# Performance work log

Hardware: AMD Instinct MI355X
Metric: run time of the kernel (lower is better)

## Reference

```python
import jax, jax.numpy as jnp
import numpy as np

TEMPERATURE = 1.0

def setup_inputs() -> dict:
    key = jax.random.key(0)
    k1, k2 = jax.random.split(key)
    B, I, O = 256, 1024, 1024
    x = jax.random.normal(k1, (B, I), dtype=jnp.float32)
    # mimic TruncatedNormal(stddev=1/sqrt(input_size)) init
    w = jax.random.normal(k2, (I, O), dtype=jnp.float32) * (1.0 / np.sqrt(I))
    b = jnp.zeros((O,), dtype=jnp.float32)
    return {"x": x, "w": w, "b": b}

def reference(x, w, b):
    # z: [B, I, O] outer product per sample
    z = jnp.einsum('bi,io->bio', x, w)
    n = x.shape[-1]
    # per-output-neuron temperature softmax over the input dim I
    s = jax.nn.softmax(jnp.abs(z) / TEMPERATURE, axis=1)
    out = n * jnp.sum(z * s, axis=1)  # [B, O]
    return out + b
```

## Files before the change

### kernel.cpp

```cpp
#include <hip/hip_runtime.h>

#define BDIM 256
#define IDIM 1024
#define ODIM 1024

#define TILE_O 64
#define TILE_B 4
#define NW 8
#define QLEN (IDIM / NW)

typedef float v2f __attribute__((ext_vector_type(2)));

#if __has_builtin(__builtin_amdgcn_exp2f)
#define FAST_EXP2(v) __builtin_amdgcn_exp2f(v)
#else
#define FAST_EXP2(v) exp2f(v)
#endif

__global__ __launch_bounds__(512, 8)
void stl_kernel(const float* __restrict__ x,
                const float* __restrict__ w,
                const float* __restrict__ bias,
                float* __restrict__ out) {
  __shared__ float xs[TILE_B][IDIM];
  __shared__ float ps[NW][TILE_O][8];

  const int tx = threadIdx.x;
  const int ty = threadIdx.y;
  const int tid = ty * 64 + tx;
  const int o0 = blockIdx.x * TILE_O;
  const int b0 = blockIdx.y * TILE_B;

  const float LOG2E = 1.4426950408889634f;

#pragma unroll
  for (int k = 0; k < 2; ++k) {
    int f = tid + k * 512;
    int row = f >> 8;
    int col = f & 255;
    float4 v = ((const float4*)(x + (size_t)(b0 + row) * IDIM))[col];
    v.x *= LOG2E; v.y *= LOG2E; v.z *= LOG2E; v.w *= LOG2E;
    ((float4*)(&xs[row][0]))[col] = v;
  }
  __syncthreads();

  const int qbase = ty * QLEN;
  const float* wp = w + (size_t)qbase * ODIM + o0 + tx;

  v2f num01 = {0.0f, 0.0f}, num23 = {0.0f, 0.0f};
  v2f den01 = {0.0f, 0.0f}, den23 = {0.0f, 0.0f};

#pragma unroll 2
  for (int j = 0; j < QLEN; j += 4) {
    float wv[4];
#pragma unroll
    for (int u = 0; u < 4; ++u) wv[u] = wp[(size_t)(j + u) * ODIM];
    float4 xq0 = *(const float4*)(&xs[0][qbase + j]);
    float4 xq1 = *(const float4*)(&xs[1][qbase + j]);
    float4 xq2 = *(const float4*)(&xs[2][qbase + j]);
    float4 xq3 = *(const float4*)(&xs[3][qbase + j]);
    const float x0[4] = {xq0.x, xq0.y, xq0.z, xq0.w};
    const float x1[4] = {xq1.x, xq1.y, xq1.z, xq1.w};
    const float x2[4] = {xq2.x, xq2.y, xq2.z, xq2.w};
    const float x3[4] = {xq3.x, xq3.y, xq3.z, xq3.w};
#pragma unroll
    for (int u = 0; u < 4; ++u) {
      v2f p01 = {x0[u] * wv[u], x1[u] * wv[u]};
      v2f p23 = {x2[u] * wv[u], x3[u] * wv[u]};
      v2f t01, t23;
      t01.x = FAST_EXP2(__builtin_fabsf(p01.x));
      t01.y = FAST_EXP2(__builtin_fabsf(p01.y));
      t23.x = FAST_EXP2(__builtin_fabsf(p23.x));
      t23.y = FAST_EXP2(__builtin_fabsf(p23.y));
      num01 += p01 * t01; den01 += t01;
      num23 += p23 * t23; den23 += t23;
    }
  }

  *(float4*)(&ps[ty][tx][0]) = make_float4(num01.x, num01.y, num23.x, num23.y);
  *(float4*)(&ps[ty][tx][4]) = make_float4(den01.x, den01.y, den23.x, den23.y);
  __syncthreads();

  if (ty == 0) {
    float n[4] = {0, 0, 0, 0}, d[4] = {0, 0, 0, 0};
#pragma unroll
    for (int q = 0; q < NW; ++q) {
      float4 a = *(const float4*)(&ps[q][tx][0]);
      float4 b = *(const float4*)(&ps[q][tx][4]);
      n[0] += a.x; n[1] += a.y; n[2] += a.z; n[3] += a.w;
      d[0] += b.x; d[1] += b.y; d[2] += b.z; d[3] += b.w;
    }
    const float LN2 = 0.6931471805599453f;
    const float scale = (float)IDIM * LN2;
    const int o = o0 + tx;
    const float bo = bias[o];
#pragma unroll
    for (int r = 0; r < 4; ++r)
      out[(size_t)(b0 + r) * ODIM + o] = scale * n[r] / d[r] + bo;
  }
}

extern "C" void kernel_launch(void* const* d_in, const int* in_sizes, int n_in,
                              void* d_out, int out_size, void* d_ws, size_t ws_size,
                              hipStream_t stream) {
  const float* x = (const float*)d_in[0];
  const float* w = (const float*)d_in[1];
  const float* b = (const float*)d_in[2];
  float* out = (float*)d_out;

  dim3 grid(ODIM / TILE_O, BDIM / TILE_B);
  dim3 block(64, NW);
  stl_kernel<<<grid, block, 0, stream>>>(x, w, b, out);
}
```

Before: 94.45 us.

## Load x via wave-uniform scalar loads and double-buffer x/w register chunks

Drops the shared-memory staging of x and its barrier. x is now read straight from global memory through a wave-uniform pointer (readfirstlane on ty), so the compiler can use scalar loads. x and w are prefetched in register double-buffered chunks of 8 to overlap loads with the exp2 compute. The LOG2E scaling moves onto w, and the packed v2f arithmetic becomes scalar floats. This raises register pressure, may lower occupancy under the 512x8 launch bound, and gives up the packed-FMA math.

```diff
diff --git a/kernel.cpp b/kernel.cpp
--- a/kernel.cpp
+++ b/kernel.cpp
@@ -8,8 +8,8 @@
 #define TILE_B 4
 #define NW 8
 #define QLEN (IDIM / NW)
-
-typedef float v2f __attribute__((ext_vector_type(2)));
+#define CHUNK 8
+#define NCHUNK (QLEN / CHUNK)
 
 #if __has_builtin(__builtin_amdgcn_exp2f)
 #define FAST_EXP2(v) __builtin_amdgcn_exp2f(v)
@@ -22,63 +22,76 @@
                 const float* __restrict__ w,
                 const float* __restrict__ bias,
                 float* __restrict__ out) {
-  __shared__ float xs[TILE_B][IDIM];
   __shared__ float ps[NW][TILE_O][8];
 
   const int tx = threadIdx.x;
   const int ty = threadIdx.y;
-  const int tid = ty * 64 + tx;
   const int o0 = blockIdx.x * TILE_O;
   const int b0 = blockIdx.y * TILE_B;
 
+  const int tyu = __builtin_amdgcn_readfirstlane(ty);
+  const int qbase = tyu * QLEN;
+
+  const float* bx = x + (size_t)b0 * IDIM + qbase;
+  const float* wp = w + (size_t)qbase * ODIM + o0 + tx;
+
   const float LOG2E = 1.4426950408889634f;
 
-#pragma unroll
-  for (int k = 0; k < 2; ++k) {
-    int f = tid + k * 512;
-    int row = f >> 8;
-    int col = f & 255;
-    float4 v = ((const float4*)(x + (size_t)(b0 + row) * IDIM))[col];
-    v.x *= LOG2E; v.y *= LOG2E; v.z *= LOG2E; v.w *= LOG2E;
-    ((float4*)(&xs[row][0]))[col] = v;
-  }
-  __syncthreads();
-
-  const int qbase = ty * QLEN;
-  const float* wp = w + (size_t)qbase * ODIM + o0 + tx;
-
-  v2f num01 = {0.0f, 0.0f}, num23 = {0.0f, 0.0f};
-  v2f den01 = {0.0f, 0.0f}, den23 = {0.0f, 0.0f};
-
-#pragma unroll 2
-  for (int j = 0; j < QLEN; j += 4) {
-    float wv[4];
-#pragma unroll
-    for (int u = 0; u < 4; ++u) wv[u] = wp[(size_t)(j + u) * ODIM];
-    float4 xq0 = *(const float4*)(&xs[0][qbase + j]);
-    float4 xq1 = *(const float4*)(&xs[1][qbase + j]);
-    float4 xq2 = *(const float4*)(&xs[2][qbase + j]);
-    float4 xq3 = *(const float4*)(&xs[3][qbase + j]);
-    const float x0[4] = {xq0.x, xq0.y, xq0.z, xq0.w};
-    const float x1[4] = {xq1.x, xq1.y, xq1.z, xq1.w};
-    const float x2[4] = {xq2.x, xq2.y, xq2.z, xq2.w};
-    const float x3[4] = {xq3.x, xq3.y, xq3.z, xq3.w};
-#pragma unroll
-    for (int u = 0; u < 4; ++u) {
-      v2f p01 = {x0[u] * wv[u], x1[u] * wv[u]};
-      v2f p23 = {x2[u] * wv[u], x3[u] * wv[u]};
-      v2f t01, t23;
-      t01.x = FAST_EXP2(__builtin_fabsf(p01.x));
-      t01.y = FAST_EXP2(__builtin_fabsf(p01.y));
-      t23.x = FAST_EXP2(__builtin_fabsf(p23.x));
-      t23.y = FAST_EXP2(__builtin_fabsf(p23.y));
-      num01 += p01 * t01; den01 += t01;
-      num23 += p23 * t23; den23 += t23;
-    }
+#define XLOAD(xdst, cc)                                                   \
+  _Pragma("unroll")                                                       \
+  for (int r = 0; r < TILE_B; ++r) {                                      \
+    _Pragma("unroll")                                                     \
+    for (int u = 0; u < CHUNK; ++u)                                       \
+      xdst[r][u] = bx[(size_t)r * IDIM + (size_t)(cc) * CHUNK + u];       \
   }
 
-  *(float4*)(&ps[ty][tx][0]) = make_float4(num01.x, num01.y, num23.x, num23.y);
-  *(float4*)(&ps[ty][tx][4]) = make_float4(den01.x, den01.y, den23.x, den23.y);
+#define WLOAD(wdst, cc)                                                   \
+  {                                                                       \
+    const float* wq = wp + (size_t)((cc) * CHUNK) * ODIM;                 \
+    _Pragma("unroll")                                                     \
+    for (int u = 0; u < CHUNK; ++u) wdst[u] = wq[(size_t)u * ODIM];       \
+  }
+
+#define COMPUTE(xc, wc)                                                   \
+  _Pragma("unroll")                                                       \
+  for (int u = 0; u < CHUNK; ++u) {                                       \
+    const float wv = wc[u] * LOG2E;         \
+    float p0 = xc[0][u] * wv;                                             \
+    float p1 = xc[1][u] * wv;                                             \
+    float p2 = xc[2][u] * wv;                                             \
+    float p3 = xc[3][u] * wv;                                             \
+    float t0 = FAST_EXP2(__builtin_fabsf(p0));      \
+    float t1 = FAST_EXP2(__builtin_fabsf(p1));                            \
+    float t2 = FAST_EXP2(__builtin_fabsf(p2));                            \
+    float t3 = FAST_EXP2(__builtin_fabsf(p3));                            \
+    num[0] += p0 * t0; den[0] += t0;                                      \
+    num[1] += p1 * t1; den[1] += t1;                                      \
+    num[2] += p2 * t2; den[2] += t2;                                      \
+    num[3] += p3 * t3; den[3] += t3;                                      \
+  }
+
+  float num[4] = {0.f, 0.f, 0.f, 0.f};
+  float den[4] = {0.f, 0.f, 0.f, 0.f};
+
+  float xA[TILE_B][CHUNK], xB[TILE_B][CHUNK];
+  float wA[CHUNK], wB[CHUNK];
+
+  XLOAD(xA, 0)
+  WLOAD(wA, 0)
+
+  for (int c = 0; c < NCHUNK; c += 2) {
+    XLOAD(xB, c + 1)
+    WLOAD(wB, c + 1)
+    COMPUTE(xA, wA)
+    if (c + 2 < NCHUNK) {
+      XLOAD(xA, c + 2)
+      WLOAD(wA, c + 2)
+    }
+    COMPUTE(xB, wB)
+  }
+
+  *(float4*)(&ps[ty][tx][0]) = make_float4(num[0], num[1], num[2], num[3]);
+  *(float4*)(&ps[ty][tx][4]) = make_float4(den[0], den[1], den[2], den[3]);
   __syncthreads();
 
   if (ty == 0) {
@@ -86,9 +99,9 @@
 #pragma unroll
     for (int q = 0; q < NW; ++q) {
       float4 a = *(const float4*)(&ps[q][tx][0]);
-      float4 b = *(const float4*)(&ps[q][tx][4]);
+      float4 b2 = *(const float4*)(&ps[q][tx][4]);
       n[0] += a.x; n[1] += a.y; n[2] += a.z; n[3] += a.w;
-      d[0] += b.x; d[1] += b.y; d[2] += b.z; d[3] += b.w;
+      d[0] += b2.x; d[1] += b2.y; d[2] += b2.z; d[3] += b2.w;
     }
     const float LN2 = 0.6931471805599453f;
     const float scale = (float)IDIM * LN2;
```

Result: slower. 101.7 us (+7.7%).
